# Performance work log

Measured on AMD Instinct MI355X. Metric: run time of the kernel, lower is better.

## Reference

```python
import jax, jax.numpy as jnp
import numpy as np

N_HEAD = 16
LN_EPS = 1e-5


def _ln(x, w, b):
    # torch LayerNorm computed in float32 then cast back (see LayerNorm.forward)
    xf = x.astype(jnp.float32)
    mu = jnp.mean(xf, axis=-1, keepdims=True)
    var = jnp.mean(jnp.square(xf - mu), axis=-1, keepdims=True)
    return ((xf - mu) * jax.lax.rsqrt(var + LN_EPS) * w + b).astype(x.dtype)


def setup_inputs() -> dict:
    key = jax.random.key(0)
    ks = jax.random.split(key, 16)
    B, S, C = 4, 1500, 1024
    A = 256  # adapter_dim
    F = 4 * C
    s = 0.02
    return {
        "x": jax.random.normal(ks[0], (B, S, C), jnp.float32),
        "Wq": jax.random.normal(ks[1], (C, C), jnp.float32) * s,
        "bq": jnp.zeros((C,), jnp.float32),
        "Wk": jax.random.normal(ks[2], (C, C), jnp.float32) * s,
        "Wv": jax.random.normal(ks[3], (C, C), jnp.float32) * s,
        "bv": jnp.zeros((C,), jnp.float32),
        "Wo": jax.random.normal(ks[4], (C, C), jnp.float32) * s,
        "bo": jnp.zeros((C,), jnp.float32),
        "ln_attn_w": jnp.ones((C,), jnp.float32),
        "ln_attn_b": jnp.zeros((C,), jnp.float32),
        "W1": jax.random.normal(ks[5], (F, C), jnp.float32) * s,
        "b1": jnp.zeros((F,), jnp.float32),
        "W2": jax.random.normal(ks[6], (C, F), jnp.float32) * s,
        "b2": jnp.zeros((C,), jnp.float32),
        "ln_mlp_w": jnp.ones((C,), jnp.float32),
        "ln_mlp_b": jnp.zeros((C,), jnp.float32),
        "Wds": jax.random.normal(ks[7], (A, C), jnp.float32) * s,
        "bds": jnp.zeros((A,), jnp.float32),
        "Wus": jax.random.normal(ks[8], (C, A), jnp.float32) * s,
        "bus": jnp.zeros((C,), jnp.float32),
    }


def reference(x, Wq, bq, Wk, Wv, bv, Wo, bo, ln_attn_w, ln_attn_b,
              W1, b1, W2, b2, ln_mlp_w, ln_mlp_b, Wds, bds, Wus, bus):
    B, S, C = x.shape
    H = N_HEAD
    D = C // H
    scale = D ** -0.25  # applied to both q and k, per qkv_attention

    # --- self-attention ---
    h = _ln(x, ln_attn_w, ln_attn_b)
    q = (h @ Wq.T + bq).reshape(B, S, H, D) * scale
    k = (h @ Wk.T).reshape(B, S, H, D) * scale  # key has no bias
    v = (h @ Wv.T + bv).reshape(B, S, H, D)
    qk = jnp.einsum("bqhd,bkhd->bhqk", q, k).astype(jnp.float32)
    w = jax.nn.softmax(qk, axis=-1).astype(x.dtype)
    wv = jnp.einsum("bhqk,bkhd->bqhd", w, v).reshape(B, S, C)
    x = x + (wv @ Wo.T + bo)

    # --- MLP (exact GELU, as nn.GELU default) ---
    h = _ln(x, ln_mlp_w, ln_mlp_b)
    x = x + (jax.nn.gelu(h @ W1.T + b1, approximate=False) @ W2.T + b2)

    # --- bottleneck adapter: x + us(gelu(ds(x))) ---
    x = x + (jax.nn.gelu(x @ Wds.T + bds, approximate=False) @ Wus.T + bus)
    return x
```

## Files before the change

### kernel.cpp

```cpp
#include <hip/hip_runtime.h>
#include <hip/hip_bf16.h>
#include <math.h>

typedef __bf16 bf16;
typedef __bf16 bf16x8 __attribute__((ext_vector_type(8)));
typedef float  f32x4  __attribute__((ext_vector_type(4)));

__device__ __forceinline__ void load16_lds(const bf16* g, bf16* l) {
    __builtin_amdgcn_global_load_lds(
        (__attribute__((address_space(1))) void*)(g),
        (__attribute__((address_space(3))) void*)(l), 16, 0, 0);
}

__device__ __forceinline__ float gelu_f(float x) {
    float u = 1.5957691216057308f * (x + 0.044715f * x * x * x);
    float e = __expf(u);
    float th = 1.0f - 2.0f / (1.0f + e);
    return 0.5f * x * (1.0f + th);
}

template<int ACT, int OMODE, class RT, class OT>
__device__ __forceinline__ void gemm_epilogue_elem(
    float v, int gm, int gn, int M, int N, float scale,
    const bf16* __restrict__ bias, const RT* __restrict__ resid,
    OT* __restrict__ out, bf16* __restrict__ out_k, bf16* __restrict__ out_v)
{
    if (bias) v += (float)bias[gn];
    if (OMODE == 2) {
        if (gn < 2048) {
            v *= scale;
            if (gn < 1024) v *= 1.4426950408889634f;
        }
    } else v *= scale;
    if (ACT == 1) v = gelu_f(v);
    if (OMODE == 2) {
        if (gn < 1024) {
            ((bf16*)out)[(size_t)gm * 1024 + gn] = (bf16)v;
        } else if (gn < 2048) {
            out_k[(size_t)gm * 1024 + (gn - 1024)] = (bf16)v;
        } else {
            int gg = gn - 2048;
            int bb = gm / 1500;
            int ss = gm - bb * 1500;
            int hh = gg >> 6, dd = gg & 63;
            out_v[(((size_t)bb * 16 + hh) * 64 + dd) * 1536 + ss] = (bf16)v;
        }
    } else {
        if (resid) v += (float)resid[(size_t)gm * N + gn];
        out[(size_t)gm * N + gn] = (OT)v;
    }
}

struct ConvArgs {
    const float* src[19];
    bf16* dst[19];
    int n[19];
    int bstart[20];
};
__global__ __launch_bounds__(256) void convert_many(ConvArgs a) {
    int blk = blockIdx.x;
    int s = 0;
    while (blk >= a.bstart[s + 1]) s++;
    const float* src = a.src[s];
    bf16* dst = a.dst[s];
    int n = a.n[s];
    int i0 = (blk - a.bstart[s]) * 2048;
#pragma unroll
    for (int e = 0; e < 8; e++) {
        int i = i0 + threadIdx.x + e * 256;
        if (i < n) dst[i] = (bf16)src[i];
    }
}

__global__ void zero_kernel(bf16* dst, int n) {
    int i = blockIdx.x * blockDim.x + threadIdx.x;
    if (i < n) dst[i] = (bf16)0.0f;
}

template<class XT>
__global__ __launch_bounds__(256) void ln_kernel(
    const XT* __restrict__ X, const bf16* __restrict__ w,
    const bf16* __restrict__ b, bf16* __restrict__ out)
{
    const int C = 1024;
    const int row = blockIdx.x;
    const int tid = threadIdx.x;
    const XT* xr = X + (size_t)row * C;
    float x0 = (float)xr[tid * 4 + 0], x1 = (float)xr[tid * 4 + 1];
    float x2 = (float)xr[tid * 4 + 2], x3 = (float)xr[tid * 4 + 3];
    float s  = x0 + x1 + x2 + x3;
    float sq = x0*x0 + x1*x1 + x2*x2 + x3*x3;
#pragma unroll
    for (int off = 32; off >= 1; off >>= 1) {
        s  += __shfl_xor(s,  off, 64);
        sq += __shfl_xor(sq, off, 64);
    }
    __shared__ float red[8];
    int wave = tid >> 6;
    if ((tid & 63) == 0) { red[wave] = s; red[4 + wave] = sq; }
    __syncthreads();
    float ts = red[0] + red[1] + red[2] + red[3];
    float tq = red[4] + red[5] + red[6] + red[7];
    float mean = ts * (1.0f / C);
    float var  = tq * (1.0f / C) - mean * mean;
    float rstd = rsqrtf(var + 1e-5f);
    float w0 = (float)w[tid*4+0], w1 = (float)w[tid*4+1], w2 = (float)w[tid*4+2], w3 = (float)w[tid*4+3];
    float b0 = (float)b[tid*4+0], b1 = (float)b[tid*4+1], b2 = (float)b[tid*4+2], b3 = (float)b[tid*4+3];
    bf16* orow = out + (size_t)row * C + tid * 4;
    orow[0] = (bf16)((x0 - mean) * rstd * w0 + b0);
    orow[1] = (bf16)((x1 - mean) * rstd * w1 + b1);
    orow[2] = (bf16)((x2 - mean) * rstd * w2 + b2);
    orow[3] = (bf16)((x3 - mean) * rstd * w3 + b3);
}

template<int ACT, int OMODE, class RT, class OT>
__global__ __launch_bounds__(256) void gemm_kernel(
    const bf16* __restrict__ A, const bf16* __restrict__ W,
    const bf16* __restrict__ bias, const RT* __restrict__ resid,
    OT* __restrict__ out, bf16* __restrict__ out_k, bf16* __restrict__ out_v,
    int M, int N, int K, float scale, int gmT, int gnT, int mQ)
{
    const int lin = blockIdx.x;
    const int xcd = lin & 7;
    const int t_  = lin >> 3;
    const int mt_ = (xcd & 3) + 4 * (t_ % mQ);
    const int nt_ = (xcd >> 2) + 2 * (t_ / mQ);
    if (mt_ >= gmT || nt_ >= gnT) return;
    const int m0 = mt_ * 128;
    const int n0 = nt_ * 128;

    __shared__ __align__(16) bf16 As[2][16 * 512];
    __shared__ __align__(16) bf16 Bs[2][16 * 512];
    const int tid = threadIdx.x;
    const int wave = tid >> 6, lane = tid & 63;
    const int lane15 = lane & 15, quad = lane >> 4;
    const int wm0 = (wave >> 1) * 64;
    const int wn0 = (wave & 1) * 64;
    f32x4 acc[4][4] = {};

    int ra0 = m0 + (2 * wave)     * 16 + lane15; if (ra0 > M - 1) ra0 = M - 1;
    int ra1 = m0 + (2 * wave + 1) * 16 + lane15; if (ra1 > M - 1) ra1 = M - 1;
    const int rb0 = n0 + (2 * wave)     * 16 + lane15;
    const int rb1 = n0 + (2 * wave + 1) * 16 + lane15;
    const bf16* a0 = A + (size_t)ra0 * K + quad * 8;
    const bf16* a1 = A + (size_t)ra1 * K + quad * 8;
    const bf16* w0 = W + (size_t)rb0 * K + quad * 8;
    const bf16* w1 = W + (size_t)rb1 * K + quad * 8;

    auto stage = [&](int buf, int k0) {
#pragma unroll
        for (int kk = 0; kk < 2; kk++) {
            load16_lds(a0 + k0 + kk * 32, &As[buf][((2 * wave)     * 2 + kk) * 512]);
            load16_lds(a1 + k0 + kk * 32, &As[buf][((2 * wave + 1) * 2 + kk) * 512]);
            load16_lds(w0 + k0 + kk * 32, &Bs[buf][((2 * wave)     * 2 + kk) * 512]);
            load16_lds(w1 + k0 + kk * 32, &Bs[buf][((2 * wave + 1) * 2 + kk) * 512]);
        }
    };

    stage(0, 0);
    asm volatile("s_waitcnt vmcnt(0)" ::: "memory");
    __builtin_amdgcn_s_barrier();
    __builtin_amdgcn_sched_barrier(0);

    const int nsteps = K >> 6;
    int cur = 0;
    for (int t = 0; t < nsteps; t++) {
        if (t + 1 < nsteps) stage(cur ^ 1, (t + 1) << 6);
#pragma unroll
        for (int kk = 0; kk < 2; kk++) {
            bf16x8 af[4], bfr[4];
#pragma unroll
            for (int tt = 0; tt < 4; tt++) {
                af[tt]  = *(const bf16x8*)(&As[cur][(((wm0 >> 4) + tt) * 2 + kk) * 512 + lane * 8]);
                bfr[tt] = *(const bf16x8*)(&Bs[cur][(((wn0 >> 4) + tt) * 2 + kk) * 512 + lane * 8]);
            }
#pragma unroll
            for (int mt = 0; mt < 4; mt++)
#pragma unroll
                for (int nt = 0; nt < 4; nt++)
                    acc[mt][nt] = __builtin_amdgcn_mfma_f32_16x16x32_bf16(
                        af[mt], bfr[nt], acc[mt][nt], 0, 0, 0);
        }
        if (t + 1 < nsteps) {
            asm volatile("s_waitcnt vmcnt(0)" ::: "memory");
            __builtin_amdgcn_s_barrier();
            __builtin_amdgcn_sched_barrier(0);
        }
        cur ^= 1;
    }

#pragma unroll
    for (int mt = 0; mt < 4; mt++) {
#pragma unroll
        for (int r = 0; r < 4; r++) {
            int gm = m0 + wm0 + mt * 16 + quad * 4 + r;
            if (gm >= M) continue;
#pragma unroll
            for (int nt = 0; nt < 4; nt++) {
                int gn = n0 + wn0 + nt * 16 + lane15;
                gemm_epilogue_elem<ACT, OMODE, RT, OT>(
                    acc[mt][nt][r], gm, gn, M, N, scale, bias, resid, out, out_k, out_v);
            }
        }
    }
}

template<int ACT, int OMODE, class RT, class OT>
__global__ __launch_bounds__(512, 2) void gemm256_kernel(
    const bf16* __restrict__ A, const bf16* __restrict__ W,
    const bf16* __restrict__ bias, const RT* __restrict__ resid,
    OT* __restrict__ out, bf16* __restrict__ out_k, bf16* __restrict__ out_v,
    int M, int N, int K, float scale, int gmT, int gnT, int mQ)
{
    const int lin = blockIdx.x;
    const int xcd = lin & 7;
    const int t_  = lin >> 3;
    const int mt_ = (xcd & 3) + 4 * (t_ % mQ);
    const int nt_ = (xcd >> 2) + 2 * (t_ / mQ);
    if (mt_ >= gmT || nt_ >= gnT) return;
    const int m0 = mt_ * 256;
    const int n0 = nt_ * 256;

    __shared__ __align__(16) bf16 As[2][32 * 512];
    __shared__ __align__(16) bf16 Bs[2][32 * 512];
    const int tid = threadIdx.x;
    const int wave = tid >> 6, lane = tid & 63;
    const int lane15 = lane & 15, quad = lane >> 4;
    const int wm0 = (wave >> 2) * 128;
    const int wn0 = (wave & 3) * 64;
    f32x4 acc[8][4] = {};

    int ra0 = m0 + (2 * wave)     * 16 + lane15; if (ra0 > M - 1) ra0 = M - 1;
    int ra1 = m0 + (2 * wave + 1) * 16 + lane15; if (ra1 > M - 1) ra1 = M - 1;
    const int rb0 = n0 + (2 * wave)     * 16 + lane15;
    const int rb1 = n0 + (2 * wave + 1) * 16 + lane15;
    const bf16* a0 = A + (size_t)ra0 * K + quad * 8;
    const bf16* a1 = A + (size_t)ra1 * K + quad * 8;
    const bf16* w0 = W + (size_t)rb0 * K + quad * 8;
    const bf16* w1 = W + (size_t)rb1 * K + quad * 8;

    auto stage = [&](int buf, int k0) {
#pragma unroll
        for (int kk = 0; kk < 2; kk++) {
            load16_lds(a0 + k0 + kk * 32, &As[buf][((2 * wave)     * 2 + kk) * 512]);
            load16_lds(a1 + k0 + kk * 32, &As[buf][((2 * wave + 1) * 2 + kk) * 512]);
            load16_lds(w0 + k0 + kk * 32, &Bs[buf][((2 * wave)     * 2 + kk) * 512]);
            load16_lds(w1 + k0 + kk * 32, &Bs[buf][((2 * wave + 1) * 2 + kk) * 512]);
        }
    };

    stage(0, 0);
    asm volatile("s_waitcnt vmcnt(0)" ::: "memory");
    __builtin_amdgcn_s_barrier();
    __builtin_amdgcn_sched_barrier(0);

    const int nsteps = K >> 6;
    int cur = 0;
    for (int t = 0; t < nsteps; t++) {
        if (t + 1 < nsteps) stage(cur ^ 1, (t + 1) << 6);
#pragma unroll
        for (int kk = 0; kk < 2; kk++) {
            bf16x8 af[8], bfr[4];
#pragma unroll
            for (int tt = 0; tt < 8; tt++)
                af[tt]  = *(const bf16x8*)(&As[cur][(((wm0 >> 4) + tt) * 2 + kk) * 512 + lane * 8]);
#pragma unroll
            for (int tt = 0; tt < 4; tt++)
                bfr[tt] = *(const bf16x8*)(&Bs[cur][(((wn0 >> 4) + tt) * 2 + kk) * 512 + lane * 8]);
#pragma unroll
            for (int mt = 0; mt < 8; mt++)
#pragma unroll
                for (int nt = 0; nt < 4; nt++)
                    acc[mt][nt] = __builtin_amdgcn_mfma_f32_16x16x32_bf16(
                        af[mt], bfr[nt], acc[mt][nt], 0, 0, 0);
        }
        if (t + 1 < nsteps) {
            asm volatile("s_waitcnt vmcnt(0)" ::: "memory");
            __builtin_amdgcn_s_barrier();
            __builtin_amdgcn_sched_barrier(0);
        }
        cur ^= 1;
    }

#pragma unroll
    for (int mt = 0; mt < 8; mt++) {
#pragma unroll
        for (int r = 0; r < 4; r++) {
            int gm = m0 + wm0 + mt * 16 + quad * 4 + r;
            if (gm >= M) continue;
#pragma unroll
            for (int nt = 0; nt < 4; nt++) {
                int gn = n0 + wn0 + nt * 16 + lane15;
                gemm_epilogue_elem<ACT, OMODE, RT, OT>(
                    acc[mt][nt][r], gm, gn, M, N, scale, bias, resid, out, out_k, out_v);
            }
        }
    }
}

__global__ __launch_bounds__(256) void flash_attn_kernel(
    const bf16* __restrict__ Q, const bf16* __restrict__ Km,
    const bf16* __restrict__ Vt, bf16* __restrict__ O)
{
    const int S = 1500, C = 1024, SP = 1536;
    const int LDP = 72;
    __shared__ __align__(16) bf16 Ks[2][8 * 512];
    __shared__ __align__(16) bf16 Vs[2][8 * 512];
    __shared__ __align__(16) bf16 Ps[4 * 16 * LDP];
    const int tid = threadIdx.x;
    const int wave = tid >> 6, lane = tid & 63;
    const int lane15 = lane & 15, quad = lane >> 4;
    const int bh = blockIdx.y;
    const int q0 = blockIdx.x * 64;
    const size_t headoff = (size_t)(bh >> 4) * S * C + (size_t)(bh & 15) * 64;
    const size_t vtoff   = (size_t)bh * 64 * SP;

    bf16x8 qf[2];
    int qr = q0 + wave * 16 + lane15; if (qr > S - 1) qr = S - 1;
    qf[0] = *(const bf16x8*)(Q + headoff + (size_t)qr * C + quad * 8);
    qf[1] = *(const bf16x8*)(Q + headoff + (size_t)qr * C + 32 + quad * 8);

    const bf16* vbase = Vt + vtoff + (size_t)(wave * 16 + lane15) * SP + quad * 8;

    auto stageKV = [&](int buf, int kt) {
        const int j0 = kt * 64;
        int kr = j0 + wave * 16 + lane15; if (kr > S - 1) kr = S - 1;
        const bf16* kbase = Km + headoff + (size_t)kr * C + quad * 8;
#pragma unroll
        for (int kk = 0; kk < 2; kk++) {
            load16_lds(kbase + kk * 32,      &Ks[buf][(wave * 2 + kk) * 512]);
            load16_lds(vbase + j0 + kk * 32, &Vs[buf][(wave * 2 + kk) * 512]);
        }
    };

    float m_run[4], l_part[4];
    f32x4 o_acc[4] = {};
#pragma unroll
    for (int r = 0; r < 4; r++) { m_run[r] = 4.0f; l_part[r] = 0.0f; }

    stageKV(0, 0);
    asm volatile("s_waitcnt vmcnt(0)" ::: "memory");
    __builtin_amdgcn_s_barrier();
    __builtin_amdgcn_sched_barrier(0);

    int cur = 0;
    for (int kt = 0; kt < 24; kt++) {
        if (kt + 1 < 24) stageKV(cur ^ 1, kt + 1);
        const int j0 = kt * 64;

        f32x4 s[4] = {};
#pragma unroll
        for (int kk = 0; kk < 2; kk++) {
#pragma unroll
            for (int nt = 0; nt < 4; nt++) {
                bf16x8 kf = *(const bf16x8*)(&Ks[cur][(nt * 2 + kk) * 512 + lane * 8]);
                s[nt] = __builtin_amdgcn_mfma_f32_16x16x32_bf16(qf[kk], kf, s[nt], 0, 0, 0);
            }
        }
        if (kt == 23) {
#pragma unroll
            for (int nt = 0; nt < 4; nt++) {
                if (j0 + nt * 16 + lane15 >= S) {
#pragma unroll
                    for (int r = 0; r < 4; r++) s[nt][r] = -1e30f;
                }
            }
        }

        float tm[4];
#pragma unroll
        for (int r = 0; r < 4; r++)
            tm[r] = fmaxf(fmaxf(s[0][r], s[1][r]), fmaxf(s[2][r], s[3][r]));
        bool rec = (tm[0] > m_run[0]) | (tm[1] > m_run[1]) |
                   (tm[2] > m_run[2]) | (tm[3] > m_run[3]);
        if (__any(rec)) {
#pragma unroll
            for (int r = 0; r < 4; r++) {
                float rm = tm[r];
#pragma unroll
                for (int off = 1; off < 16; off <<= 1) rm = fmaxf(rm, __shfl_xor(rm, off, 64));
                float mnew  = fmaxf(m_run[r], rm);
                float alpha = __builtin_amdgcn_exp2f(m_run[r] - mnew);
                m_run[r] = mnew;
                l_part[r] *= alpha;
#pragma unroll
                for (int dt = 0; dt < 4; dt++) o_acc[dt][r] *= alpha;
            }
        }

#pragma unroll
        for (int nt = 0; nt < 4; nt++) {
#pragma unroll
            for (int r = 0; r < 4; r++) {
                float p = __builtin_amdgcn_exp2f(s[nt][r] - m_run[r]);
                l_part[r] += p;
                Ps[wave * 16 * LDP + (quad * 4 + r) * LDP + nt * 16 + lane15] = (bf16)p;
            }
        }
        asm volatile("s_waitcnt lgkmcnt(0)" ::: "memory");
        __builtin_amdgcn_sched_barrier(0);
#pragma unroll
        for (int kk = 0; kk < 2; kk++) {
            bf16x8 pf = *(const bf16x8*)(&Ps[wave * 16 * LDP + lane15 * LDP + kk * 32 + quad * 8]);
#pragma unroll
            for (int dt = 0; dt < 4; dt++) {
                bf16x8 vf = *(const bf16x8*)(&Vs[cur][(dt * 2 + kk) * 512 + lane * 8]);
                o_acc[dt] = __builtin_amdgcn_mfma_f32_16x16x32_bf16(pf, vf, o_acc[dt], 0, 0, 0);
            }
        }
        if (kt + 1 < 24) {
            asm volatile("s_waitcnt vmcnt(0)" ::: "memory");
            __builtin_amdgcn_s_barrier();
            __builtin_amdgcn_sched_barrier(0);
        }
        cur ^= 1;
    }

    float l_inv[4];
#pragma unroll
    for (int r = 0; r < 4; r++) {
        float ls = l_part[r];
#pragma unroll
        for (int off = 1; off < 16; off <<= 1) ls += __shfl_xor(ls, off, 64);
        l_inv[r] = 1.0f / ls;
    }

#pragma unroll
    for (int dt = 0; dt < 4; dt++) {
#pragma unroll
        for (int r = 0; r < 4; r++) {
            int row = q0 + wave * 16 + quad * 4 + r;
            if (row < S) {
                float v = o_acc[dt][r] * l_inv[r];
                O[headoff + (size_t)row * C + dt * 16 + lane15] = (bf16)v;
            }
        }
    }
}

extern "C" void kernel_launch(void* const* d_in, const int* in_sizes, int n_in,
                              void* d_out, int out_size, void* d_ws, size_t ws_size,
                              hipStream_t stream) {
    float* out = (float*)d_out;
    const float* x_f32 = (const float*)d_in[0];
    const int M = 6000, Cc = 1024, F = 4096, Aa = 256;
    const size_t MC = (size_t)M * Cc;
    const size_t VT_ELEMS = (size_t)64 * 64 * 1536;
    bf16* ws = (bf16*)d_ws;

    bf16* h1   = ws;
    bf16* kbuf = ws + MC;
    bf16* Vt   = ws + 2 * MC;
    bf16* g    = ws + 2 * MC + VT_ELEMS;
    bf16* q    = (bf16*)d_out;
    bf16* wv   = h1;
    bf16* x1   = q;
    bf16* h2   = kbuf;
    bf16* x2   = Vt;
    bf16* aact = kbuf;

    size_t off = 2 * MC + VT_ELEMS + (size_t)M * F;
    bf16* Wqkv = ws + off; off += (size_t)3 * 1024 * 1024;
    bf16* bqkv = ws + off; off += 3072;
    bf16* sWo  = ws + off; off += (size_t)1024 * 1024;
    bf16* sbo  = ws + off; off += 1024;
    bf16* slnw = ws + off; off += 1024;
    bf16* slnb = ws + off; off += 1024;
    bf16* sW1  = ws + off; off += (size_t)4096 * 1024;
    bf16* sb1  = ws + off; off += 4096;
    bf16* sW2  = ws + off; off += (size_t)1024 * 4096;
    bf16* sb2  = ws + off; off += 1024;
    bf16* sln2w = ws + off; off += 1024;
    bf16* sln2b = ws + off; off += 1024;
    bf16* sWds = ws + off; off += (size_t)256 * 1024;
    bf16* sbds = ws + off; off += 256;
    bf16* sWus = ws + off; off += (size_t)1024 * 256;
    bf16* sbus = ws + off; off += 1024;

    ConvArgs ca;
    const int srcidx[19] = {1, 3, 4, 2, 5, 6, 7, 8, 9, 10, 11, 12, 13, 14, 15, 16, 17, 18, 19};
    bf16* dsts[19] = {Wqkv, Wqkv + 1048576, Wqkv + 2097152, bqkv, bqkv + 2048,
                      sWo, sbo, slnw, slnb, sW1, sb1, sW2, sb2, sln2w, sln2b,
                      sWds, sbds, sWus, sbus};
    int bacc = 0;
    for (int i = 0; i < 19; i++) {
        ca.src[i] = (const float*)d_in[srcidx[i]];
        ca.dst[i] = dsts[i];
        ca.n[i] = in_sizes[srcidx[i]];
        ca.bstart[i] = bacc;
        bacc += (ca.n[i] + 2047) / 2048;
    }
    ca.bstart[19] = bacc;

    dim3 blk(256);
    dim3 blk512(512);
    convert_many<<<bacc, blk, 0, stream>>>(ca);
    zero_kernel<<<4, blk, 0, stream>>>(bqkv + 1024, 1024);

    const float scale = 0.35355339059327373f;
    const int gmT = 47, mQ = 12;
    auto grid_for = [&](int gnT) { int nQ = (gnT + 1) >> 1; return dim3(8 * mQ * nQ); };
    const int gmT2 = 24, mQ2 = 6;
    auto grid256_for = [&](int gnT) { int nQ = (gnT + 1) >> 1; return dim3(8 * mQ2 * nQ); };

    ln_kernel<float><<<M, blk, 0, stream>>>(x_f32, slnw, slnb, h1);
    gemm256_kernel<0, 2, bf16, bf16><<<grid256_for(12), blk512, 0, stream>>>(
        h1, Wqkv, bqkv, (const bf16*)nullptr, q, kbuf, Vt, M, 3072, Cc, scale, gmT2, 12, mQ2);
    dim3 ga(24, 64);
    flash_attn_kernel<<<ga, blk, 0, stream>>>(q, kbuf, Vt, wv);
    gemm_kernel<0, 0, float, bf16><<<grid_for(8), blk, 0, stream>>>(
        wv, sWo, sbo, x_f32, x1, nullptr, nullptr, M, Cc, Cc, 1.0f, gmT, 8, mQ);
    ln_kernel<bf16><<<M, blk, 0, stream>>>(x1, sln2w, sln2b, h2);
    gemm256_kernel<1, 0, bf16, bf16><<<grid256_for(16), blk512, 0, stream>>>(
        h2, sW1, sb1, (const bf16*)nullptr, g, nullptr, nullptr, M, F, Cc, 1.0f, gmT2, 16, mQ2);
    gemm_kernel<0, 0, bf16, bf16><<<grid_for(8), blk, 0, stream>>>(
        g, sW2, sb2, x1, x2, nullptr, nullptr, M, Cc, F, 1.0f, gmT, 8, mQ);
    gemm_kernel<1, 0, bf16, bf16><<<grid_for(2), blk, 0, stream>>>(
        x2, sWds, sbds, (const bf16*)nullptr, aact, nullptr, nullptr, M, Aa, Cc, 1.0f, gmT, 2, mQ);
    gemm_kernel<0, 0, bf16, float><<<grid_for(8), blk, 0, stream>>>(
        aact, sWus, sbus, x2, out, nullptr, nullptr, M, Cc, Aa, 1.0f, gmT, 8, mQ);
}
```

Baseline: 849.1 us.

## Restructure large GEMM mainloop into phased ping-pong schedule with priority hints

The 256x256-style GEMM mainloop is split into four phases, each issuing part of the next tile's global-to-LDS prefetch and its own LDS fragment loads, then running a block of MFMAs raised with s_setprio, with barriers between phases. This aims to interleave memory traffic with matrix math and coordinate waves in ping-pong fashion. Separately, the 128x128 GEMM drops double buffering for a single LDS buffer with __syncthreads, halving its LDS footprint to raise occupancy at the cost of exposing load latency. The extra barriers per step add sync overhead.

Result: no change. 852.0 us (+0.3%).

```diff
diff --git a/kernel.cpp b/kernel.cpp
--- a/kernel.cpp
+++ b/kernel.cpp
@@ -129,8 +129,8 @@
     const int m0 = mt_ * 128;
     const int n0 = nt_ * 128;
 
-    __shared__ __align__(16) bf16 As[2][16 * 512];
-    __shared__ __align__(16) bf16 Bs[2][16 * 512];
+    __shared__ __align__(16) bf16 As[16 * 512];
+    __shared__ __align__(16) bf16 Bs[16 * 512];
     const int tid = threadIdx.x;
     const int wave = tid >> 6, lane = tid & 63;
     const int lane15 = lane & 15, quad = lane >> 4;
@@ -147,32 +147,22 @@
     const bf16* w0 = W + (size_t)rb0 * K + quad * 8;
     const bf16* w1 = W + (size_t)rb1 * K + quad * 8;
 
-    auto stage = [&](int buf, int k0) {
-#pragma unroll
-        for (int kk = 0; kk < 2; kk++) {
-            load16_lds(a0 + k0 + kk * 32, &As[buf][((2 * wave)     * 2 + kk) * 512]);
-            load16_lds(a1 + k0 + kk * 32, &As[buf][((2 * wave + 1) * 2 + kk) * 512]);
-            load16_lds(w0 + k0 + kk * 32, &Bs[buf][((2 * wave)     * 2 + kk) * 512]);
-            load16_lds(w1 + k0 + kk * 32, &Bs[buf][((2 * wave + 1) * 2 + kk) * 512]);
-        }
-    };
-
-    stage(0, 0);
-    asm volatile("s_waitcnt vmcnt(0)" ::: "memory");
-    __builtin_amdgcn_s_barrier();
-    __builtin_amdgcn_sched_barrier(0);
-
-    const int nsteps = K >> 6;
-    int cur = 0;
-    for (int t = 0; t < nsteps; t++) {
-        if (t + 1 < nsteps) stage(cur ^ 1, (t + 1) << 6);
+    for (int k0 = 0; k0 < K; k0 += 64) {
+#pragma unroll
+        for (int kk = 0; kk < 2; kk++) {
+            load16_lds(a0 + k0 + kk * 32, &As[((2 * wave)     * 2 + kk) * 512]);
+            load16_lds(a1 + k0 + kk * 32, &As[((2 * wave + 1) * 2 + kk) * 512]);
+            load16_lds(w0 + k0 + kk * 32, &Bs[((2 * wave)     * 2 + kk) * 512]);
+            load16_lds(w1 + k0 + kk * 32, &Bs[((2 * wave + 1) * 2 + kk) * 512]);
+        }
+        __syncthreads();
 #pragma unroll
         for (int kk = 0; kk < 2; kk++) {
             bf16x8 af[4], bfr[4];
 #pragma unroll
             for (int tt = 0; tt < 4; tt++) {
-                af[tt]  = *(const bf16x8*)(&As[cur][(((wm0 >> 4) + tt) * 2 + kk) * 512 + lane * 8]);
-                bfr[tt] = *(const bf16x8*)(&Bs[cur][(((wn0 >> 4) + tt) * 2 + kk) * 512 + lane * 8]);
+                af[tt]  = *(const bf16x8*)(&As[(((wm0 >> 4) + tt) * 2 + kk) * 512 + lane * 8]);
+                bfr[tt] = *(const bf16x8*)(&Bs[(((wn0 >> 4) + tt) * 2 + kk) * 512 + lane * 8]);
             }
 #pragma unroll
             for (int mt = 0; mt < 4; mt++)
@@ -181,12 +171,7 @@
                     acc[mt][nt] = __builtin_amdgcn_mfma_f32_16x16x32_bf16(
                         af[mt], bfr[nt], acc[mt][nt], 0, 0, 0);
         }
-        if (t + 1 < nsteps) {
-            asm volatile("s_waitcnt vmcnt(0)" ::: "memory");
-            __builtin_amdgcn_s_barrier();
-            __builtin_amdgcn_sched_barrier(0);
-        }
-        cur ^= 1;
+        __syncthreads();
     }
 
 #pragma unroll
@@ -239,47 +224,94 @@
     const bf16* w0 = W + (size_t)rb0 * K + quad * 8;
     const bf16* w1 = W + (size_t)rb1 * K + quad * 8;
 
-    auto stage = [&](int buf, int k0) {
+    auto stageA = [&](int buf, int k0) {
 #pragma unroll
         for (int kk = 0; kk < 2; kk++) {
             load16_lds(a0 + k0 + kk * 32, &As[buf][((2 * wave)     * 2 + kk) * 512]);
             load16_lds(a1 + k0 + kk * 32, &As[buf][((2 * wave + 1) * 2 + kk) * 512]);
+        }
+    };
+    auto stageB = [&](int buf, int k0) {
+#pragma unroll
+        for (int kk = 0; kk < 2; kk++) {
             load16_lds(w0 + k0 + kk * 32, &Bs[buf][((2 * wave)     * 2 + kk) * 512]);
             load16_lds(w1 + k0 + kk * 32, &Bs[buf][((2 * wave + 1) * 2 + kk) * 512]);
         }
     };
-
-    stage(0, 0);
+    auto LDA = [&](int buf, int i, int kk) -> bf16x8 {
+        return *(const bf16x8*)(&As[buf][(((wm0 >> 4) + i) * 2 + kk) * 512 + lane * 8]);
+    };
+    auto LDB = [&](int buf, int j, int kk) -> bf16x8 {
+        return *(const bf16x8*)(&Bs[buf][(((wn0 >> 4) + j) * 2 + kk) * 512 + lane * 8]);
+    };
+
+    stageA(0, 0); stageB(0, 0);
     asm volatile("s_waitcnt vmcnt(0)" ::: "memory");
     __builtin_amdgcn_s_barrier();
     __builtin_amdgcn_sched_barrier(0);
 
     const int nsteps = K >> 6;
-    int cur = 0;
     for (int t = 0; t < nsteps; t++) {
-        if (t + 1 < nsteps) stage(cur ^ 1, (t + 1) << 6);
-#pragma unroll
-        for (int kk = 0; kk < 2; kk++) {
-            bf16x8 af[8], bfr[4];
-#pragma unroll
-            for (int tt = 0; tt < 8; tt++)
-                af[tt]  = *(const bf16x8*)(&As[cur][(((wm0 >> 4) + tt) * 2 + kk) * 512 + lane * 8]);
-#pragma unroll
-            for (int tt = 0; tt < 4; tt++)
-                bfr[tt] = *(const bf16x8*)(&Bs[cur][(((wn0 >> 4) + tt) * 2 + kk) * 512 + lane * 8]);
-#pragma unroll
-            for (int mt = 0; mt < 8; mt++)
-#pragma unroll
-                for (int nt = 0; nt < 4; nt++)
-                    acc[mt][nt] = __builtin_amdgcn_mfma_f32_16x16x32_bf16(
-                        af[mt], bfr[nt], acc[mt][nt], 0, 0, 0);
-        }
-        if (t + 1 < nsteps) {
-            asm volatile("s_waitcnt vmcnt(0)" ::: "memory");
-            __builtin_amdgcn_s_barrier();
-            __builtin_amdgcn_sched_barrier(0);
-        }
-        cur ^= 1;
+        const int cur = t & 1, nxt = cur ^ 1;
+        const bool pf = (t + 1 < nsteps);
+        const int k1 = (t + 1) << 6;
+        bf16x8 af[8], bfr[2];
+
+#pragma unroll
+        for (int i = 0; i < 8; i++) af[i] = LDA(cur, i, 0);
+        bfr[0] = LDB(cur, 0, 0); bfr[1] = LDB(cur, 1, 0);
+        if (pf) stageA(nxt, k1);
+        asm volatile("s_waitcnt lgkmcnt(0)" ::: "memory");
+        __builtin_amdgcn_sched_barrier(0);
+        __builtin_amdgcn_s_setprio(1);
+#pragma unroll
+        for (int mt = 0; mt < 8; mt++)
+#pragma unroll
+            for (int j = 0; j < 2; j++)
+                acc[mt][j] = __builtin_amdgcn_mfma_f32_16x16x32_bf16(af[mt], bfr[j], acc[mt][j], 0, 0, 0);
+        __builtin_amdgcn_s_setprio(0);
+        __builtin_amdgcn_s_barrier();
+
+        bfr[0] = LDB(cur, 2, 0); bfr[1] = LDB(cur, 3, 0);
+        if (pf) stageB(nxt, k1);
+        asm volatile("s_waitcnt lgkmcnt(0)" ::: "memory");
+        __builtin_amdgcn_sched_barrier(0);
+        __builtin_amdgcn_s_setprio(1);
+#pragma unroll
+        for (int mt = 0; mt < 8; mt++)
+#pragma unroll
+            for (int j = 0; j < 2; j++)
+                acc[mt][2 + j] = __builtin_amdgcn_mfma_f32_16x16x32_bf16(af[mt], bfr[j], acc[mt][2 + j], 0, 0, 0);
+        __builtin_amdgcn_s_setprio(0);
+        __builtin_amdgcn_s_barrier();
+
+#pragma unroll
+        for (int i = 0; i < 8; i++) af[i] = LDA(cur, i, 1);
+        bfr[0] = LDB(cur, 0, 1); bfr[1] = LDB(cur, 1, 1);
+        asm volatile("s_waitcnt lgkmcnt(0)" ::: "memory");
+        __builtin_amdgcn_sched_barrier(0);
+        __builtin_amdgcn_s_setprio(1);
+#pragma unroll
+        for (int mt = 0; mt < 8; mt++)
+#pragma unroll
+            for (int j = 0; j < 2; j++)
+                acc[mt][j] = __builtin_amdgcn_mfma_f32_16x16x32_bf16(af[mt], bfr[j], acc[mt][j], 0, 0, 0);
+        __builtin_amdgcn_s_setprio(0);
+        __builtin_amdgcn_s_barrier();
+
+        bfr[0] = LDB(cur, 2, 1); bfr[1] = LDB(cur, 3, 1);
+        asm volatile("s_waitcnt lgkmcnt(0)" ::: "memory");
+        __builtin_amdgcn_sched_barrier(0);
+        __builtin_amdgcn_s_setprio(1);
+#pragma unroll
+        for (int mt = 0; mt < 8; mt++)
+#pragma unroll
+            for (int j = 0; j < 2; j++)
+                acc[mt][2 + j] = __builtin_amdgcn_mfma_f32_16x16x32_bf16(af[mt], bfr[j], acc[mt][2 + j], 0, 0, 0);
+        __builtin_amdgcn_s_setprio(0);
+        if (pf) asm volatile("s_waitcnt vmcnt(0)" ::: "memory");
+        __builtin_amdgcn_s_barrier();
+        __builtin_amdgcn_sched_barrier(0);
     }
 
 #pragma unroll
```
